# Optimization experiments

Hardware: AMD Instinct MI355X
Metric: run time of the kernel (lower is better)

The kernel has to match this reference:

```python
import jax, jax.numpy as jnp
import numpy as np

N_NODES = 100000
N_EDGES = 1600000
D_IN = 128
D_HID = 128
N_CLS = 2


def gcn_conv(x, edge_index, W, b):
    """PyG GCNConv: add self-loops, symmetric normalization, linear, scatter-add, bias."""
    n = x.shape[0]
    loop = jnp.arange(n, dtype=edge_index.dtype)
    src = jnp.concatenate([edge_index[0], loop])  # [E+N]
    dst = jnp.concatenate([edge_index[1], loop])
    # degree computed on destination (col) after adding self-loops
    deg = jax.ops.segment_sum(jnp.ones_like(dst, dtype=x.dtype), dst, num_segments=n)
    dinv = jnp.where(deg > 0, jax.lax.rsqrt(deg), 0.0)
    norm = dinv[src] * dinv[dst]  # [E+N]
    h = x @ W  # [N, out]
    msg = h[src] * norm[:, None]  # [E+N, out]
    out = jax.ops.segment_sum(msg, dst, num_segments=n)
    return out + b


def setup_inputs() -> dict:
    key = jax.random.key(0)
    k1, k2, k3, k4 = jax.random.split(key, 4)
    x = jax.random.normal(k1, (N_NODES, D_IN), dtype=jnp.float32)
    edge_index = jax.random.randint(k2, (2, N_EDGES), 0, N_NODES, dtype=jnp.int64)
    W1 = jax.random.normal(k3, (D_IN, D_HID), dtype=jnp.float32) * (1.0 / np.sqrt(D_IN))
    b1 = jnp.zeros((D_HID,), dtype=jnp.float32)
    W2 = jax.random.normal(k4, (D_HID, N_CLS), dtype=jnp.float32) * (1.0 / np.sqrt(D_HID))
    b2 = jnp.zeros((N_CLS,), dtype=jnp.float32)
    return {"x": x, "edge_index": edge_index, "W1": W1, "b1": b1, "W2": W2, "b2": b2}


def reference(x, edge_index, W1, b1, W2, b2):
    h = gcn_conv(x, edge_index, W1, b1)
    h = jax.nn.relu(h)
    # training=False -> dropout skipped
    out = gcn_conv(h, edge_index, W2, b2)
    return out
```

## Files before the change

kernel.cpp:

```cpp
#include <hip/hip_runtime.h>
#include <hip/hip_fp16.h>
#include <cstdint>
#include <cstddef>

#define NN 100000
#define NE 1600000
#define D 128
#define NBK 782
#define NBLK_P 200
#define EPB 8000

typedef _Float16 half8 __attribute__((ext_vector_type(8)));
typedef _Float16 half4v __attribute__((ext_vector_type(4)));
typedef float f32x4 __attribute__((ext_vector_type(4)));


__launch_bounds__(256)
__global__ void p1_count_k(const int* __restrict__ ei, unsigned* __restrict__ offs,
                           const float* __restrict__ W, _Float16* __restrict__ Wt) {
    __shared__ unsigned hist[NBK];
    int tid = threadIdx.x, b = blockIdx.x;
    for (int k = tid; k < NBK; k += 256) hist[k] = 0u;
    __syncthreads();
    int e0 = b * EPB;
    for (int i = tid * 4; i < EPB; i += 1024) {
        int4 d4 = *(const int4*)(ei + NE + e0 + i);
        atomicAdd(&hist[d4.x >> 7], 1u);
        atomicAdd(&hist[d4.y >> 7], 1u);
        atomicAdd(&hist[d4.z >> 7], 1u);
        atomicAdd(&hist[d4.w >> 7], 1u);
    }
    __syncthreads();
    for (int k = tid; k < NBK; k += 256) offs[(size_t)b * NBK + k] = hist[k];

    if (b < 64) {
        int idx = b * 256 + tid;
        int n = idx >> 7, k = idx & 127;
        Wt[idx] = (_Float16)W[k * 128 + n];
    }
}

__launch_bounds__(256)
__global__ void p2a_k(unsigned* __restrict__ offs, unsigned* __restrict__ base) {
    __shared__ unsigned sh[256];
    int t = threadIdx.x, k = blockIdx.x;
    unsigned v = (t < NBLK_P) ? offs[(size_t)t * NBK + k] : 0u;
    sh[t] = v;
    __syncthreads();
    for (int off = 1; off < 256; off <<= 1) {
        unsigned u = (t >= off) ? sh[t - off] : 0u;
        __syncthreads();
        sh[t] += u;
        __syncthreads();
    }
    if (t < NBLK_P) offs[(size_t)t * NBK + k] = sh[t] - v;
    if (t == 255) base[k] = sh[255];
}

__global__ void p2b_k(unsigned* __restrict__ base) {
    __shared__ unsigned sh[1024];
    int t = threadIdx.x;
    unsigned v = (t < NBK) ? base[t] : 0u;
    sh[t] = v;
    __syncthreads();
    for (int off = 1; off < 1024; off <<= 1) {
        unsigned u = (t >= off) ? sh[t - off] : 0u;
        __syncthreads();
        sh[t] += u;
        __syncthreads();
    }
    if (t < NBK) base[t] = sh[t] - v;
    if (t == NBK) base[NBK] = sh[NBK - 1];
}

__launch_bounds__(256)
__global__ void p3_scatter_k(const int* __restrict__ ei, const unsigned* __restrict__ offs,
                             const unsigned* __restrict__ base, unsigned* __restrict__ part) {
    __shared__ unsigned lcnt[NBK];
    int tid = threadIdx.x, b = blockIdx.x;
    for (int k = tid; k < NBK; k += 256) lcnt[k] = base[k] + offs[(size_t)b * NBK + k];
    __syncthreads();
    int e0 = b * EPB;
    for (int i = tid * 4; i < EPB; i += 1024) {
        int4 s4 = *(const int4*)(ei + e0 + i);
        int4 d4 = *(const int4*)(ei + NE + e0 + i);
        unsigned p;
        p = atomicAdd(&lcnt[d4.x >> 7], 1u); part[p] = (unsigned)s4.x | ((unsigned)(d4.x & 127) << 20);
        p = atomicAdd(&lcnt[d4.y >> 7], 1u); part[p] = (unsigned)s4.y | ((unsigned)(d4.y & 127) << 20);
        p = atomicAdd(&lcnt[d4.z >> 7], 1u); part[p] = (unsigned)s4.z | ((unsigned)(d4.z & 127) << 20);
        p = atomicAdd(&lcnt[d4.w >> 7], 1u); part[p] = (unsigned)s4.w | ((unsigned)(d4.w & 127) << 20);
    }
}

__launch_bounds__(256)
__global__ void p4_csr_k(const unsigned* __restrict__ part, const unsigned* __restrict__ base,
                         unsigned* __restrict__ rp, float* __restrict__ dinv,
                         unsigned* __restrict__ col) {
    __shared__ unsigned c[128], p[128], run[128];
    int tid = threadIdx.x, k = blockIdx.x;
    int n0 = k << 7;
    int nodes = (NN - n0 < 128) ? (NN - n0) : 128;
    unsigned e0 = base[k], e1 = base[k + 1];

    if (tid < 128) c[tid] = 0u;
    __syncthreads();
    for (unsigned e = e0 + tid; e < e1; e += 256)
        atomicAdd(&c[(part[e] >> 20) & 127], 1u);
    __syncthreads();

    unsigned myc = (tid < 128) ? c[tid] : 0u;
    if (tid < 128) p[tid] = myc;
    __syncthreads();
    for (int off = 1; off < 128; off <<= 1) {
        unsigned u = 0;
        if (tid < 128 && tid >= off) u = p[tid - off];
        __syncthreads();
        if (tid < 128) p[tid] += u;
        __syncthreads();
    }
    if (tid < 128) {
        unsigned excl = p[tid] - myc;
        run[tid] = excl;
        if (tid < nodes) {
            rp[n0 + tid] = e0 + excl;
            dinv[n0 + tid] = rsqrtf((float)(myc + 1u));
        }
    }
    if (k == 0 && tid == 0) rp[NN] = NE;
    __syncthreads();

    for (unsigned e = e0 + tid; e < e1; e += 256) {
        unsigned v = part[e];
        unsigned dlo = (v >> 20) & 127;
        unsigned pos = e0 + atomicAdd(&run[dlo], 1u);
        col[pos] = v & 0xFFFFFu;
    }
}

__launch_bounds__(256)
__global__ void gemm1_k(const float* __restrict__ x, const _Float16* __restrict__ Wt,
                        const float* __restrict__ dinv, _Float16* __restrict__ h) {
    __shared__ _Float16 wt[128 * 136];
    __shared__ _Float16 xs[128 * 72];
    int tid = threadIdx.x;
    int rb = blockIdx.x * 128;
    int w = tid >> 6, lane = tid & 63;
    int m = lane & 15, q4 = lane >> 4;

#pragma unroll
    for (int q = 0; q < 8; q++) {
        int idx = q * 256 + tid;
        int n = idx >> 4, k8 = (idx & 15) * 8;
        *(half8*)(&wt[n * 136 + k8]) = *(const half8*)(Wt + n * 128 + k8);
    }

    f32x4 acc[2][8];
#pragma unroll
    for (int rt = 0; rt < 2; rt++)
#pragma unroll
        for (int nt = 0; nt < 8; nt++) acc[rt][nt] = (f32x4){0.f, 0.f, 0.f, 0.f};

    for (int ks = 0; ks <= 64; ks += 64) {
        if (ks) __syncthreads();
#pragma unroll
        for (int q = 0; q < 8; q++) {
            int idx = q * 256 + tid;
            int row = idx >> 4;
            int c4 = (idx & 15) * 4;
            int gr = rb + row;
            float4 v = (gr < NN) ? *(const float4*)(x + (size_t)gr * 128 + ks + c4)
                                 : make_float4(0, 0, 0, 0);
            half4v hv = { (_Float16)v.x, (_Float16)v.y, (_Float16)v.z, (_Float16)v.w };
            *(half4v*)(&xs[row * 72 + c4]) = hv;
        }
        __syncthreads();

#pragma unroll
        for (int kc = 0; kc < 2; kc++) {
            half8 a0 = *(const half8*)(&xs[(w * 32 + m) * 72 + kc * 32 + q4 * 8]);
            half8 a1 = *(const half8*)(&xs[(w * 32 + 16 + m) * 72 + kc * 32 + q4 * 8]);
#pragma unroll
            for (int nt = 0; nt < 8; nt++) {
                half8 bf = *(const half8*)(&wt[(nt * 16 + m) * 136 + ks + kc * 32 + q4 * 8]);
                acc[0][nt] = __builtin_amdgcn_mfma_f32_16x16x32_f16(a0, bf, acc[0][nt], 0, 0, 0);
                acc[1][nt] = __builtin_amdgcn_mfma_f32_16x16x32_f16(a1, bf, acc[1][nt], 0, 0, 0);
            }
        }
    }

    float dv[2][4];
#pragma unroll
    for (int rt = 0; rt < 2; rt++)
#pragma unroll
        for (int r = 0; r < 4; r++) {
            int ri = rb + w * 32 + rt * 16 + q4 * 4 + r;
            dv[rt][r] = (ri < NN) ? dinv[ri] : 0.f;
        }
    __syncthreads();
#pragma unroll
    for (int rt = 0; rt < 2; rt++)
#pragma unroll
        for (int nt = 0; nt < 8; nt++)
#pragma unroll
            for (int r = 0; r < 4; r++)
                wt[(w * 32 + rt * 16 + q4 * 4 + r) * 136 + nt * 16 + m] =
                    (_Float16)(acc[rt][nt][r] * dv[rt][r]);
    __syncthreads();
#pragma unroll
    for (int q = 0; q < 8; q++) {
        int idx = q * 256 + tid;
        int row = idx >> 4;
        int c8 = (idx & 15) * 8;
        int gr = rb + row;
        if (gr < NN)
            *(half8*)(h + (size_t)gr * 128 + c8) = *(const half8*)(&wt[row * 136 + c8]);
    }
}

#define GATHER(sv, vv) \
    { unsigned s_ = __builtin_amdgcn_readfirstlane(col[sv]); \
      vv = __half22float2(hb[(size_t)(s_ * 64u + lane)]); }

__launch_bounds__(256)
__global__ void agg1_k(const _Float16* __restrict__ h, const unsigned* __restrict__ rp,
                       const unsigned* __restrict__ col, const float* __restrict__ dinv,
                       const float* __restrict__ b1, const float* __restrict__ W2,
                       float* __restrict__ z) {
    int i = (blockIdx.x * 256 + threadIdx.x) >> 6;
    int lane = threadIdx.x & 63;
    if (i >= NN) return;

    const __half2* hb = (const __half2*)h;
    float di = dinv[i];
    float2 hv = __half22float2(hb[(size_t)i * 64 + lane]);
    float ax = hv.x, ay = hv.y;

    unsigned p0 = __builtin_amdgcn_readfirstlane(rp[i]);
    unsigned p1 = __builtin_amdgcn_readfirstlane(rp[i + 1]);
    unsigned e = p0;
    for (; e + 16 <= p1; e += 16) {
        float2 v0, v1, v2, v3, v4, v5, v6, v7, v8, v9, va, vb, vc, vd, ve, vf;
        GATHER(e, v0)      GATHER(e + 1, v1)  GATHER(e + 2, v2)  GATHER(e + 3, v3)
        GATHER(e + 4, v4)  GATHER(e + 5, v5)  GATHER(e + 6, v6)  GATHER(e + 7, v7)
        GATHER(e + 8, v8)  GATHER(e + 9, v9)  GATHER(e + 10, va) GATHER(e + 11, vb)
        GATHER(e + 12, vc) GATHER(e + 13, vd) GATHER(e + 14, ve) GATHER(e + 15, vf)
        ax += ((v0.x + v1.x) + (v2.x + v3.x)) + ((v4.x + v5.x) + (v6.x + v7.x))
            + ((v8.x + v9.x) + (va.x + vb.x)) + ((vc.x + vd.x) + (ve.x + vf.x));
        ay += ((v0.y + v1.y) + (v2.y + v3.y)) + ((v4.y + v5.y) + (v6.y + v7.y))
            + ((v8.y + v9.y) + (va.y + vb.y)) + ((vc.y + vd.y) + (ve.y + vf.y));
    }
    for (; e + 4 <= p1; e += 4) {
        float2 v0, v1, v2, v3;
        GATHER(e, v0) GATHER(e + 1, v1) GATHER(e + 2, v2) GATHER(e + 3, v3)
        ax += (v0.x + v1.x) + (v2.x + v3.x);
        ay += (v0.y + v1.y) + (v2.y + v3.y);
    }
    for (; e < p1; ++e) {
        float2 v;
        GATHER(e, v)
        ax += v.x;
        ay += v.y;
    }
    ax *= di;
    ay *= di;

    float2 bv = ((const float2*)b1)[lane];
    float h0 = fmaxf(ax + bv.x, 0.f);
    float h1 = fmaxf(ay + bv.y, 0.f);

    float4 w = ((const float4*)W2)[lane];
    float pz0 = fmaf(h0, w.x, h1 * w.z);
    float pz1 = fmaf(h0, w.y, h1 * w.w);
#pragma unroll
    for (int off = 32; off > 0; off >>= 1) {
        pz0 += __shfl_down(pz0, off);
        pz1 += __shfl_down(pz1, off);
    }
    if (lane == 0) {
        float2* zp = (float2*)(z + (size_t)i * 2);
        *zp = make_float2(pz0 * di, pz1 * di);
    }
}

__launch_bounds__(256)
__global__ void agg2_k(const float* __restrict__ z, const unsigned* __restrict__ rp,
                       const unsigned* __restrict__ col, const float* __restrict__ dinv,
                       const float* __restrict__ b2, float* __restrict__ out) {
    int i = (blockIdx.x * 256 + threadIdx.x) >> 4;
    int sl = threadIdx.x & 15;
    if (i >= NN) return;

    unsigned p0 = rp[i], p1 = rp[i + 1];
    float a0 = 0.f, a1 = 0.f;
    for (unsigned e = p0 + sl; e < p1; e += 16) {
        unsigned s = col[e];
        float2 v = ((const float2*)z)[s];
        a0 += v.x;
        a1 += v.y;
    }
#pragma unroll
    for (int off = 8; off > 0; off >>= 1) {
        a0 += __shfl_down(a0, off, 16);
        a1 += __shfl_down(a1, off, 16);
    }
    if (sl == 0) {
        float di = dinv[i];
        float2 zi = ((const float2*)z)[i];
        out[(size_t)i * 2]     = (a0 + zi.x) * di + b2[0];
        out[(size_t)i * 2 + 1] = (a1 + zi.y) * di + b2[1];
    }
}

extern "C" void kernel_launch(void* const* d_in, const int* in_sizes, int n_in,
                              void* d_out, int out_size, void* d_ws, size_t ws_size,
                              hipStream_t stream) {
    const float* x  = (const float*)d_in[0];
    const int*   ei = (const int*)d_in[1];
    const float* W1 = (const float*)d_in[2];
    const float* b1 = (const float*)d_in[3];
    const float* W2 = (const float*)d_in[4];
    const float* b2 = (const float*)d_in[5];
    float* out = (float*)d_out;

    char* ws = (char*)d_ws;
    unsigned* part = (unsigned*)(ws);
    unsigned* offs = (unsigned*)(ws + 6400000);
    unsigned* base = (unsigned*)(ws + 7100000);
    _Float16* h    = (_Float16*)(ws);
    float*    z    = (float*)(ws + 25600000);
    float*    dinv = (float*)(ws + 26400000);
    unsigned* rp   = (unsigned*)(ws + 26800000);
    unsigned* col  = (unsigned*)(ws + 27200016);
    _Float16* Wt   = (_Float16*)(ws + 33600016);

    p1_count_k<<<NBLK_P, 256, 0, stream>>>(ei, offs, W1, Wt);
    p2a_k<<<NBK, 256, 0, stream>>>(offs, base);
    p2b_k<<<1, 1024, 0, stream>>>(base);
    p3_scatter_k<<<NBLK_P, 256, 0, stream>>>(ei, offs, base, part);
    p4_csr_k<<<NBK, 256, 0, stream>>>(part, base, rp, dinv, col);

    gemm1_k<<<(NN + 127) / 128, 256, 0, stream>>>(x, Wt, dinv, h);
    agg1_k<<<(NN + 3) / 4, 256, 0, stream>>>(h, rp, col, dinv, b1, W2, z);
    agg2_k<<<(NN * 16 + 255) / 256, 256, 0, stream>>>(z, rp, col, dinv, b2, out);
}
```

Measured before the change: 223.9 us.

## Fuse CSR build phases into one cooperative kernel with grid syncs

Replaces the five CSR-construction kernels (count, two scans, scatter, per-bucket sort) with a single cooperative kernel of 256 blocks of 1024 threads, separated by grid.sync barriers. The goal is to remove four kernel launches and their inter-kernel gaps. In exchange, scalar loads replace int4 vector loads, the second scan runs on one block while the rest wait, and each block processes several buckets in a loop. The base buffer is moved so it still fits after the larger offs array.

```diff
diff --git a/kernel.cpp b/kernel.cpp
--- a/kernel.cpp
+++ b/kernel.cpp
@@ -1,139 +1,143 @@
 #include <hip/hip_runtime.h>
 #include <hip/hip_fp16.h>
+#include <hip/hip_cooperative_groups.h>
 #include <cstdint>
 #include <cstddef>
+
+namespace cg = cooperative_groups;
 
 #define NN 100000
 #define NE 1600000
 #define D 128
 #define NBK 782
-#define NBLK_P 200
-#define EPB 8000
+#define NCHK 256
+#define ECH 6250
 
 typedef _Float16 half8 __attribute__((ext_vector_type(8)));
 typedef _Float16 half4v __attribute__((ext_vector_type(4)));
 typedef float f32x4 __attribute__((ext_vector_type(4)));
 
 
-__launch_bounds__(256)
-__global__ void p1_count_k(const int* __restrict__ ei, unsigned* __restrict__ offs,
-                           const float* __restrict__ W, _Float16* __restrict__ Wt) {
-    __shared__ unsigned hist[NBK];
+__launch_bounds__(1024)
+__global__ void csr_k(const int* __restrict__ ei,
+                      unsigned* __restrict__ offs, unsigned* __restrict__ base,
+                      unsigned* __restrict__ part,
+                      unsigned* __restrict__ rp, float* __restrict__ dinv,
+                      unsigned* __restrict__ col,
+                      const float* __restrict__ W, _Float16* __restrict__ Wt) {
+    cg::grid_group grid = cg::this_grid();
+    __shared__ unsigned smem[1024];
     int tid = threadIdx.x, b = blockIdx.x;
-    for (int k = tid; k < NBK; k += 256) hist[k] = 0u;
-    __syncthreads();
-    int e0 = b * EPB;
-    for (int i = tid * 4; i < EPB; i += 1024) {
-        int4 d4 = *(const int4*)(ei + NE + e0 + i);
-        atomicAdd(&hist[d4.x >> 7], 1u);
-        atomicAdd(&hist[d4.y >> 7], 1u);
-        atomicAdd(&hist[d4.z >> 7], 1u);
-        atomicAdd(&hist[d4.w >> 7], 1u);
-    }
-    __syncthreads();
-    for (int k = tid; k < NBK; k += 256) offs[(size_t)b * NBK + k] = hist[k];
-
-    if (b < 64) {
-        int idx = b * 256 + tid;
+
+    for (int k = tid; k < NBK; k += 1024) smem[k] = 0u;
+    __syncthreads();
+    {
+        int e0 = b * ECH;
+        for (int i = tid; i < ECH; i += 1024) {
+            int d = ei[NE + e0 + i];
+            atomicAdd(&smem[d >> 7], 1u);
+        }
+    }
+    if (b < 16) {
+        int idx = b * 1024 + tid;
         int n = idx >> 7, k = idx & 127;
         Wt[idx] = (_Float16)W[k * 128 + n];
     }
-}
-
-__launch_bounds__(256)
-__global__ void p2a_k(unsigned* __restrict__ offs, unsigned* __restrict__ base) {
-    __shared__ unsigned sh[256];
-    int t = threadIdx.x, k = blockIdx.x;
-    unsigned v = (t < NBLK_P) ? offs[(size_t)t * NBK + k] : 0u;
-    sh[t] = v;
-    __syncthreads();
-    for (int off = 1; off < 256; off <<= 1) {
-        unsigned u = (t >= off) ? sh[t - off] : 0u;
-        __syncthreads();
-        sh[t] += u;
-        __syncthreads();
-    }
-    if (t < NBLK_P) offs[(size_t)t * NBK + k] = sh[t] - v;
-    if (t == 255) base[k] = sh[255];
-}
-
-__global__ void p2b_k(unsigned* __restrict__ base) {
-    __shared__ unsigned sh[1024];
-    int t = threadIdx.x;
-    unsigned v = (t < NBK) ? base[t] : 0u;
-    sh[t] = v;
-    __syncthreads();
-    for (int off = 1; off < 1024; off <<= 1) {
-        unsigned u = (t >= off) ? sh[t - off] : 0u;
-        __syncthreads();
-        sh[t] += u;
-        __syncthreads();
-    }
-    if (t < NBK) base[t] = sh[t] - v;
-    if (t == NBK) base[NBK] = sh[NBK - 1];
-}
-
-__launch_bounds__(256)
-__global__ void p3_scatter_k(const int* __restrict__ ei, const unsigned* __restrict__ offs,
-                             const unsigned* __restrict__ base, unsigned* __restrict__ part) {
-    __shared__ unsigned lcnt[NBK];
-    int tid = threadIdx.x, b = blockIdx.x;
-    for (int k = tid; k < NBK; k += 256) lcnt[k] = base[k] + offs[(size_t)b * NBK + k];
-    __syncthreads();
-    int e0 = b * EPB;
-    for (int i = tid * 4; i < EPB; i += 1024) {
-        int4 s4 = *(const int4*)(ei + e0 + i);
-        int4 d4 = *(const int4*)(ei + NE + e0 + i);
-        unsigned p;
-        p = atomicAdd(&lcnt[d4.x >> 7], 1u); part[p] = (unsigned)s4.x | ((unsigned)(d4.x & 127) << 20);
-        p = atomicAdd(&lcnt[d4.y >> 7], 1u); part[p] = (unsigned)s4.y | ((unsigned)(d4.y & 127) << 20);
-        p = atomicAdd(&lcnt[d4.z >> 7], 1u); part[p] = (unsigned)s4.z | ((unsigned)(d4.z & 127) << 20);
-        p = atomicAdd(&lcnt[d4.w >> 7], 1u); part[p] = (unsigned)s4.w | ((unsigned)(d4.w & 127) << 20);
-    }
-}
-
-__launch_bounds__(256)
-__global__ void p4_csr_k(const unsigned* __restrict__ part, const unsigned* __restrict__ base,
-                         unsigned* __restrict__ rp, float* __restrict__ dinv,
-                         unsigned* __restrict__ col) {
-    __shared__ unsigned c[128], p[128], run[128];
-    int tid = threadIdx.x, k = blockIdx.x;
-    int n0 = k << 7;
-    int nodes = (NN - n0 < 128) ? (NN - n0) : 128;
-    unsigned e0 = base[k], e1 = base[k + 1];
-
-    if (tid < 128) c[tid] = 0u;
-    __syncthreads();
-    for (unsigned e = e0 + tid; e < e1; e += 256)
-        atomicAdd(&c[(part[e] >> 20) & 127], 1u);
-    __syncthreads();
-
-    unsigned myc = (tid < 128) ? c[tid] : 0u;
-    if (tid < 128) p[tid] = myc;
-    __syncthreads();
-    for (int off = 1; off < 128; off <<= 1) {
-        unsigned u = 0;
-        if (tid < 128 && tid >= off) u = p[tid - off];
-        __syncthreads();
-        if (tid < 128) p[tid] += u;
-        __syncthreads();
-    }
-    if (tid < 128) {
-        unsigned excl = p[tid] - myc;
-        run[tid] = excl;
-        if (tid < nodes) {
-            rp[n0 + tid] = e0 + excl;
-            dinv[n0 + tid] = rsqrtf((float)(myc + 1u));
-        }
-    }
-    if (k == 0 && tid == 0) rp[NN] = NE;
-    __syncthreads();
-
-    for (unsigned e = e0 + tid; e < e1; e += 256) {
-        unsigned v = part[e];
-        unsigned dlo = (v >> 20) & 127;
-        unsigned pos = e0 + atomicAdd(&run[dlo], 1u);
-        col[pos] = v & 0xFFFFFu;
+    __syncthreads();
+    for (int k = tid; k < NBK; k += 1024) offs[(size_t)b * NBK + k] = smem[k];
+    __threadfence();
+    grid.sync();
+
+    {
+        int g = tid >> 8, t8 = tid & 255;
+        int k = b + (g << 8);
+        unsigned v = (k < NBK) ? offs[(size_t)t8 * NBK + k] : 0u;
+        unsigned* sh = &smem[g << 8];
+        sh[t8] = v;
+        __syncthreads();
+        for (int off = 1; off < 256; off <<= 1) {
+            unsigned u = (t8 >= off) ? sh[t8 - off] : 0u;
+            __syncthreads();
+            sh[t8] += u;
+            __syncthreads();
+        }
+        if (k < NBK) {
+            offs[(size_t)t8 * NBK + k] = sh[t8] - v;
+            if (t8 == 255) base[k] = sh[255];
+        }
+    }
+    __threadfence();
+    grid.sync();
+
+    if (b == 0) {
+        unsigned v = (tid < NBK) ? base[tid] : 0u;
+        smem[tid] = v;
+        __syncthreads();
+        for (int off = 1; off < 1024; off <<= 1) {
+            unsigned u = (tid >= off) ? smem[tid - off] : 0u;
+            __syncthreads();
+            smem[tid] += u;
+            __syncthreads();
+        }
+        if (tid < NBK) base[tid] = smem[tid] - v;
+        if (tid == NBK) base[NBK] = smem[NBK - 1];
+        if (tid == 0) rp[NN] = NE;
+        __threadfence();
+    }
+    grid.sync();
+
+    for (int k = tid; k < NBK; k += 1024) smem[k] = base[k] + offs[(size_t)b * NBK + k];
+    __syncthreads();
+    {
+        int e0 = b * ECH;
+        for (int i = tid; i < ECH; i += 1024) {
+            int s = ei[e0 + i];
+            int d = ei[NE + e0 + i];
+            unsigned pos = atomicAdd(&smem[d >> 7], 1u);
+            part[pos] = (unsigned)s | ((unsigned)(d & 127) << 20);
+        }
+    }
+    __threadfence();
+    grid.sync();
+
+    unsigned* c = smem; unsigned* pp = smem + 128; unsigned* run = smem + 256;
+    for (int kk = b; kk < NBK; kk += NCHK) {
+        int n0 = kk << 7;
+        int nodes = (NN - n0 < 128) ? (NN - n0) : 128;
+        unsigned e0 = base[kk], e1 = base[kk + 1];
+
+        if (tid < 128) c[tid] = 0u;
+        __syncthreads();
+        for (unsigned e = e0 + tid; e < e1; e += 1024)
+            atomicAdd(&c[(part[e] >> 20) & 127], 1u);
+        __syncthreads();
+
+        unsigned myc = (tid < 128) ? c[tid] : 0u;
+        if (tid < 128) pp[tid] = myc;
+        __syncthreads();
+        for (int off = 1; off < 128; off <<= 1) {
+            unsigned u = 0;
+            if (tid < 128 && tid >= off) u = pp[tid - off];
+            __syncthreads();
+            if (tid < 128) pp[tid] += u;
+            __syncthreads();
+        }
+        if (tid < 128) {
+            unsigned excl = pp[tid] - myc;
+            run[tid] = excl;
+            if (tid < nodes) {
+                rp[n0 + tid] = e0 + excl;
+                dinv[n0 + tid] = rsqrtf((float)(myc + 1u));
+            }
+        }
+        __syncthreads();
+        for (unsigned e = e0 + tid; e < e1; e += 1024) {
+            unsigned v = part[e];
+            unsigned dlo = (v >> 20) & 127;
+            unsigned pos = e0 + atomicAdd(&run[dlo], 1u);
+            col[pos] = v & 0xFFFFFu;
+        }
+        __syncthreads();
     }
 }
 
@@ -325,7 +329,7 @@
     char* ws = (char*)d_ws;
     unsigned* part = (unsigned*)(ws);
     unsigned* offs = (unsigned*)(ws + 6400000);
-    unsigned* base = (unsigned*)(ws + 7100000);
+    unsigned* base = (unsigned*)(ws + 7300000);
     _Float16* h    = (_Float16*)(ws);
     float*    z    = (float*)(ws + 25600000);
     float*    dinv = (float*)(ws + 26400000);
@@ -333,11 +337,9 @@
     unsigned* col  = (unsigned*)(ws + 27200016);
     _Float16* Wt   = (_Float16*)(ws + 33600016);
 
-    p1_count_k<<<NBLK_P, 256, 0, stream>>>(ei, offs, W1, Wt);
-    p2a_k<<<NBK, 256, 0, stream>>>(offs, base);
-    p2b_k<<<1, 1024, 0, stream>>>(base);
-    p3_scatter_k<<<NBLK_P, 256, 0, stream>>>(ei, offs, base, part);
-    p4_csr_k<<<NBK, 256, 0, stream>>>(part, base, rp, dinv, col);
+    void* args[] = { (void*)&ei, (void*)&offs, (void*)&base, (void*)&part,
+                     (void*)&rp, (void*)&dinv, (void*)&col, (void*)&W1, (void*)&Wt };
+    hipLaunchCooperativeKernel((void*)csr_k, dim3(NCHK), dim3(1024), args, 0, stream);
 
     gemm1_k<<<(NN + 127) / 128, 256, 0, stream>>>(x, Wt, dinv, h);
     agg1_k<<<(NN + 3) / 4, 256, 0, stream>>>(h, rp, col, dinv, b1, W2, z);
```

Result: slower. 660.6 us (+195.0%).

## Replace two-pass bucket sort with fixed-capacity bucket scatter via global atomics

Applied to the files above, without the earlier changes.

The count, two-level scan and scatter passes used to bucket edges by destination block are replaced by one scatter kernel. It appends each edge into a fixed-capacity slot region per bucket (CAP entries) using global atomic counters, then runs a small scan over bucket counts. The finish kernel reads each bucket's contiguous region and builds CSR as before. This removes a full pass over the edge list and two kernel launches, but adds contention on global atomics. It would overflow silently if any bucket receives more than CAP edges, which holds only for roughly uniform random degree distributions.

```diff
diff --git a/kernel.cpp b/kernel.cpp
--- a/kernel.cpp
+++ b/kernel.cpp
@@ -7,8 +7,7 @@
 #define NE 1600000
 #define D 128
 #define NBK 782
-#define NBLK_P 200
-#define EPB 8000
+#define CAP 2560
 
 typedef _Float16 half8 __attribute__((ext_vector_type(8)));
 typedef _Float16 half4v __attribute__((ext_vector_type(4)));
@@ -16,51 +15,34 @@
 
 
 __launch_bounds__(256)
-__global__ void p1_count_k(const int* __restrict__ ei, unsigned* __restrict__ offs,
-                           const float* __restrict__ W, _Float16* __restrict__ Wt) {
-    __shared__ unsigned hist[NBK];
-    int tid = threadIdx.x, b = blockIdx.x;
-    for (int k = tid; k < NBK; k += 256) hist[k] = 0u;
-    __syncthreads();
-    int e0 = b * EPB;
-    for (int i = tid * 4; i < EPB; i += 1024) {
-        int4 d4 = *(const int4*)(ei + NE + e0 + i);
-        atomicAdd(&hist[d4.x >> 7], 1u);
-        atomicAdd(&hist[d4.y >> 7], 1u);
-        atomicAdd(&hist[d4.z >> 7], 1u);
-        atomicAdd(&hist[d4.w >> 7], 1u);
-    }
-    __syncthreads();
-    for (int k = tid; k < NBK; k += 256) offs[(size_t)b * NBK + k] = hist[k];
-
-    if (b < 64) {
-        int idx = b * 256 + tid;
+__global__ void scatter_k(const int* __restrict__ ei, unsigned* __restrict__ gcnt,
+                          unsigned* __restrict__ part,
+                          const float* __restrict__ W, _Float16* __restrict__ Wt) {
+    int i = (blockIdx.x * 256 + threadIdx.x) * 4;
+    if (blockIdx.x < 64) {
+        int idx = blockIdx.x * 256 + threadIdx.x;
         int n = idx >> 7, k = idx & 127;
         Wt[idx] = (_Float16)W[k * 128 + n];
     }
-}
-
-__launch_bounds__(256)
-__global__ void p2a_k(unsigned* __restrict__ offs, unsigned* __restrict__ base) {
-    __shared__ unsigned sh[256];
-    int t = threadIdx.x, k = blockIdx.x;
-    unsigned v = (t < NBLK_P) ? offs[(size_t)t * NBK + k] : 0u;
-    sh[t] = v;
-    __syncthreads();
-    for (int off = 1; off < 256; off <<= 1) {
-        unsigned u = (t >= off) ? sh[t - off] : 0u;
-        __syncthreads();
-        sh[t] += u;
-        __syncthreads();
-    }
-    if (t < NBLK_P) offs[(size_t)t * NBK + k] = sh[t] - v;
-    if (t == 255) base[k] = sh[255];
-}
-
-__global__ void p2b_k(unsigned* __restrict__ base) {
+    if (i >= NE) return;
+    int4 s4 = *(const int4*)(ei + i);
+    int4 d4 = *(const int4*)(ei + NE + i);
+    unsigned b, p;
+    b = (unsigned)d4.x >> 7; p = atomicAdd(&gcnt[b], 1u);
+    part[b * CAP + p] = (unsigned)s4.x | ((unsigned)(d4.x & 127) << 20);
+    b = (unsigned)d4.y >> 7; p = atomicAdd(&gcnt[b], 1u);
+    part[b * CAP + p] = (unsigned)s4.y | ((unsigned)(d4.y & 127) << 20);
+    b = (unsigned)d4.z >> 7; p = atomicAdd(&gcnt[b], 1u);
+    part[b * CAP + p] = (unsigned)s4.z | ((unsigned)(d4.z & 127) << 20);
+    b = (unsigned)d4.w >> 7; p = atomicAdd(&gcnt[b], 1u);
+    part[b * CAP + p] = (unsigned)s4.w | ((unsigned)(d4.w & 127) << 20);
+}
+
+__global__ void scan_k(const unsigned* __restrict__ gcnt, unsigned* __restrict__ base,
+                       unsigned* __restrict__ rp) {
     __shared__ unsigned sh[1024];
     int t = threadIdx.x;
-    unsigned v = (t < NBK) ? base[t] : 0u;
+    unsigned v = (t < NBK) ? gcnt[t] : 0u;
     sh[t] = v;
     __syncthreads();
     for (int off = 1; off < 1024; off <<= 1) {
@@ -71,41 +53,26 @@
     }
     if (t < NBK) base[t] = sh[t] - v;
     if (t == NBK) base[NBK] = sh[NBK - 1];
-}
-
-__launch_bounds__(256)
-__global__ void p3_scatter_k(const int* __restrict__ ei, const unsigned* __restrict__ offs,
-                             const unsigned* __restrict__ base, unsigned* __restrict__ part) {
-    __shared__ unsigned lcnt[NBK];
-    int tid = threadIdx.x, b = blockIdx.x;
-    for (int k = tid; k < NBK; k += 256) lcnt[k] = base[k] + offs[(size_t)b * NBK + k];
-    __syncthreads();
-    int e0 = b * EPB;
-    for (int i = tid * 4; i < EPB; i += 1024) {
-        int4 s4 = *(const int4*)(ei + e0 + i);
-        int4 d4 = *(const int4*)(ei + NE + e0 + i);
-        unsigned p;
-        p = atomicAdd(&lcnt[d4.x >> 7], 1u); part[p] = (unsigned)s4.x | ((unsigned)(d4.x & 127) << 20);
-        p = atomicAdd(&lcnt[d4.y >> 7], 1u); part[p] = (unsigned)s4.y | ((unsigned)(d4.y & 127) << 20);
-        p = atomicAdd(&lcnt[d4.z >> 7], 1u); part[p] = (unsigned)s4.z | ((unsigned)(d4.z & 127) << 20);
-        p = atomicAdd(&lcnt[d4.w >> 7], 1u); part[p] = (unsigned)s4.w | ((unsigned)(d4.w & 127) << 20);
-    }
-}
-
-__launch_bounds__(256)
-__global__ void p4_csr_k(const unsigned* __restrict__ part, const unsigned* __restrict__ base,
-                         unsigned* __restrict__ rp, float* __restrict__ dinv,
-                         unsigned* __restrict__ col) {
+    if (t == 0) rp[NN] = NE;
+}
+
+__launch_bounds__(256)
+__global__ void fin_k(const unsigned* __restrict__ part, const unsigned* __restrict__ gcnt,
+                      const unsigned* __restrict__ base,
+                      unsigned* __restrict__ rp, float* __restrict__ dinv,
+                      unsigned* __restrict__ col) {
     __shared__ unsigned c[128], p[128], run[128];
     int tid = threadIdx.x, k = blockIdx.x;
     int n0 = k << 7;
     int nodes = (NN - n0 < 128) ? (NN - n0) : 128;
-    unsigned e0 = base[k], e1 = base[k + 1];
+    unsigned cnt = gcnt[k];
+    unsigned e0 = base[k];
+    const unsigned* src = part + (size_t)k * CAP;
 
     if (tid < 128) c[tid] = 0u;
     __syncthreads();
-    for (unsigned e = e0 + tid; e < e1; e += 256)
-        atomicAdd(&c[(part[e] >> 20) & 127], 1u);
+    for (unsigned e = tid; e < cnt; e += 256)
+        atomicAdd(&c[(src[e] >> 20) & 127], 1u);
     __syncthreads();
 
     unsigned myc = (tid < 128) ? c[tid] : 0u;
@@ -126,11 +93,10 @@
             dinv[n0 + tid] = rsqrtf((float)(myc + 1u));
         }
     }
-    if (k == 0 && tid == 0) rp[NN] = NE;
-    __syncthreads();
-
-    for (unsigned e = e0 + tid; e < e1; e += 256) {
-        unsigned v = part[e];
+    __syncthreads();
+
+    for (unsigned e = tid; e < cnt; e += 256) {
+        unsigned v = src[e];
         unsigned dlo = (v >> 20) & 127;
         unsigned pos = e0 + atomicAdd(&run[dlo], 1u);
         col[pos] = v & 0xFFFFFu;
@@ -324,8 +290,8 @@
 
     char* ws = (char*)d_ws;
     unsigned* part = (unsigned*)(ws);
-    unsigned* offs = (unsigned*)(ws + 6400000);
-    unsigned* base = (unsigned*)(ws + 7100000);
+    unsigned* gcnt = (unsigned*)(ws + 8100000);
+    unsigned* base = (unsigned*)(ws + 8110000);
     _Float16* h    = (_Float16*)(ws);
     float*    z    = (float*)(ws + 25600000);
     float*    dinv = (float*)(ws + 26400000);
@@ -333,11 +299,10 @@
     unsigned* col  = (unsigned*)(ws + 27200016);
     _Float16* Wt   = (_Float16*)(ws + 33600016);
 
-    p1_count_k<<<NBLK_P, 256, 0, stream>>>(ei, offs, W1, Wt);
-    p2a_k<<<NBK, 256, 0, stream>>>(offs, base);
-    p2b_k<<<1, 1024, 0, stream>>>(base);
-    p3_scatter_k<<<NBLK_P, 256, 0, stream>>>(ei, offs, base, part);
-    p4_csr_k<<<NBK, 256, 0, stream>>>(part, base, rp, dinv, col);
+    hipMemsetAsync(gcnt, 0, NBK * sizeof(unsigned), stream);
+    scatter_k<<<(NE / 4 + 255) / 256, 256, 0, stream>>>(ei, gcnt, part, W1, Wt);
+    scan_k<<<1, 1024, 0, stream>>>(gcnt, base, rp);
+    fin_k<<<NBK, 256, 0, stream>>>(part, gcnt, base, rp, dinv, col);
 
     gemm1_k<<<(NN + 127) / 128, 256, 0, stream>>>(x, Wt, dinv, h);
     agg1_k<<<(NN + 3) / 4, 256, 0, stream>>>(h, rp, col, dinv, b1, W2, z);
```

Result: slower. 585.0 us (+161.2%).
